# Kernel optimization log

Measured on AMD Instinct MI355X. Metric: run time of the kernel, lower is better.

Reference implementation:

```python
import jax, jax.numpy as jnp
import numpy as np

F = 16  # ConvLSTM2D filters

def hard_sigmoid(x):
    # Keras (TF2) hard_sigmoid: clip(0.2*x + 0.5, 0, 1) -- ConvLSTM2D default recurrent_activation
    return jnp.clip(0.2 * x + 0.5, 0.0, 1.0)

def convlstm_1x1(x, W, U, b, reverse):
    # x: [B,T,H,W,C]; W: [C,4F]; U: [F,4F]; b: [4F]
    # 1x1 ConvLSTM2D == per-pixel LSTM; gate order in Keras kernel: i, f, c, o
    B, T, H, Wd, C = x.shape
    xs = jnp.moveaxis(x, 1, 0)  # [T,B,H,W,C]
    h0 = jnp.zeros((B, H, Wd, F), x.dtype)
    c0 = jnp.zeros((B, H, Wd, F), x.dtype)
    def step(carry, xt):
        h, c = carry
        z = jnp.einsum('bhwc,cf->bhwf', xt, W) + jnp.einsum('bhwc,cf->bhwf', h, U) + b
        i, f, g, o = jnp.split(z, 4, axis=-1)
        i = hard_sigmoid(i); f = hard_sigmoid(f); o = hard_sigmoid(o)
        c_new = f * c + i * jnp.tanh(g)
        h_new = o * jnp.tanh(c_new)
        return (h_new, c_new), h_new
    # reverse=True: scan runs backward in time, ys aligned to input order,
    # which matches Keras Bidirectional(go_backwards + output re-reversal).
    _, hs = jax.lax.scan(step, (h0, c0), xs, reverse=reverse)
    return jnp.moveaxis(hs, 0, 1)  # [B,T,H,W,F]

def setup_inputs() -> dict:
    key = jax.random.key(0)
    ks = jax.random.split(key, 13)
    B, T, H, Wd, C = 16, 64, 32, 32, 32
    s = 0.1
    inp = {
        'inputs': jax.random.normal(ks[0], (B, T, H, Wd, C), jnp.float32),
        'Wf': jax.random.normal(ks[1], (C, 4 * F), jnp.float32) * s,
        'Uf': jax.random.normal(ks[2], (F, 4 * F), jnp.float32) * s,
        'bf': jnp.zeros((4 * F,), jnp.float32),
        'Wb': jax.random.normal(ks[3], (C, 4 * F), jnp.float32) * s,
        'Ub': jax.random.normal(ks[4], (F, 4 * F), jnp.float32) * s,
        'bb': jnp.zeros((4 * F,), jnp.float32),
        'w1': jax.random.normal(ks[5], (2 * F, 16), jnp.float32) * s,
        'b1': jnp.zeros((16,), jnp.float32),
        'w2': jax.random.normal(ks[6], (16, 16), jnp.float32) * s,
        'b2': jnp.zeros((16,), jnp.float32),
        'w3': jax.random.normal(ks[7], (16, 10), jnp.float32) * s,
        'b3': jnp.zeros((10,), jnp.float32),
    }
    return inp

def reference(inputs, Wf, Uf, bf, Wb, Ub, bb, w1, b1, w2, b2, w3, b3):
    h_fwd = convlstm_1x1(inputs, Wf, Uf, bf, reverse=False)
    h_bwd = convlstm_1x1(inputs, Wb, Ub, bb, reverse=True)
    x = jnp.concatenate([h_fwd, h_bwd], axis=-1)  # [B,T,H,W,2F]
    x = jnp.einsum('...c,cd->...d', x, w1) + b1
    x = jnp.einsum('...c,cd->...d', x, w2) + b2
    x = jnp.einsum('...c,cd->...d', x, w3) + b3
    return x  # [B,T,H,W,10]
```

## Files before the change

kernel.cpp:

```cpp
#include <hip/hip_runtime.h>
#include <hip/hip_bf16.h>
#include <cstdint>
#include <cstddef>

#define TT 64
#define CC 32
#define FF 16
#define HWSZ 1024
#define NPIX 16384

typedef __attribute__((ext_vector_type(8))) short  short8;
typedef __attribute__((ext_vector_type(4))) float  f32x4;

__device__ __forceinline__ float bf2f(unsigned int u16) {
  union { unsigned int u; float f; } c;
  c.u = u16 << 16;
  return c.f;
}
__device__ __forceinline__ unsigned int f2bf(float f) {
  union { float f; unsigned int u; } c;
  c.f = f;
  unsigned int u = c.u;
  return (u + 0x7fffu + ((u >> 16) & 1u)) >> 16;
}
__device__ __forceinline__ unsigned int pkbf(float a, float b) {
  float2 f2; f2.x = a; f2.y = b;
  __hip_bfloat162 h = __float22bfloat162_rn(f2);
  union { __hip_bfloat162 h; unsigned int u; } c; c.h = h;
  return c.u;
}
__device__ __forceinline__ float clamp01(float x) {
  return fminf(fmaxf(x, 0.0f), 1.0f);
}

#define L2E2 2.8853900817779268f
__device__ __forceinline__ float tanh_e2(float e2arg) {
  const float e = __builtin_exp2f(e2arg);
  const float t = __builtin_amdgcn_rcpf(e + 1.0f);
  return fmaf(-2.0f, t, 1.0f);
}

__global__ __launch_bounds__(512) void fold_kernel(
    const float* __restrict__ w1, const float* __restrict__ b1,
    const float* __restrict__ w2, const float* __restrict__ b2,
    const float* __restrict__ w3, const float* __restrict__ b3,
    float* __restrict__ Wc, float* __restrict__ bc)
{
  __shared__ float w23[16 * 10];
  __shared__ float bb2[16];
  const int t = threadIdx.x;

  if (t < 160) {
    const int k = t / 10, j = t % 10;
    float s = 0.0f;
    #pragma unroll
    for (int m = 0; m < 16; ++m) s = fmaf(w2[k * 16 + m], w3[m * 10 + j], s);
    w23[t] = s;
  }
  if (t < 16) {
    float s = b2[t];
    #pragma unroll
    for (int m = 0; m < 16; ++m) s = fmaf(b1[m], w2[m * 16 + t], s);
    bb2[t] = s;
  }
  __syncthreads();
  if (t < 320) {
    const int k = t / 10, j = t % 10;
    float s = 0.0f;
    #pragma unroll
    for (int m = 0; m < 16; ++m) s = fmaf(w1[k * 16 + m], w23[m * 10 + j], s);
    Wc[t] = s;
  }
  if (t < 10) {
    float s = b3[t];
    #pragma unroll
    for (int m = 0; m < 16; ++m) s = fmaf(bb2[m], w3[m * 10 + t], s);
    bc[t] = s;
  }
}

__global__ __launch_bounds__(256) void lstm_kernel(
    const float* __restrict__ x,
    const float* __restrict__ Wf, const float* __restrict__ Uf, const float* __restrict__ bfp,
    const float* __restrict__ Wb, const float* __restrict__ Ub, const float* __restrict__ bbp,
    unsigned short* __restrict__ hf_out, unsigned short* __restrict__ hb_out)
{
  const int dir = blockIdx.y;
  const float* __restrict__ Wp = dir ? Wb : Wf;
  const float* __restrict__ Up = dir ? Ub : Uf;
  const float* __restrict__ bp = dir ? bbp : bfp;
  unsigned short* __restrict__ hout = dir ? hb_out : hf_out;

  const int tid  = threadIdx.x;
  const int lane = tid & 63;
  const int wid  = tid >> 6;
  const int quad = lane >> 4;
  const int l15  = lane & 15;

  __shared__ unsigned short hst[4 * 16 * 40];
  unsigned short* hwv = hst + wid * 16 * 40;
  for (int i = tid; i < 4 * 16 * 40; i += 256) hst[i] = 0;
  __syncthreads();

  const int px  = (blockIdx.x * 4 + wid) * 16 + l15;
  const int b   = px >> 10;
  const int hwi = px & 1023;

  short8 Bx[4], Bu[4];
  #pragma unroll
  for (int nt = 0; nt < 4; ++nt) {
    short8 vx, vu;
    #pragma unroll
    for (int j = 0; j < 8; ++j) {
      const int k   = quad * 8 + j;
      const int col = nt * 16 + l15;
      vx[j] = (short)f2bf(Wp[k * 64 + col]);
      vu[j] = (k < FF) ? (short)f2bf(Up[k * 64 + col]) : (short)0;
    }
    Bx[nt] = vx; Bu[nt] = vu;
  }
  const float bi  = fmaf(bp[ 0 + l15], 0.2f, 0.5f);
  const float bf  = fmaf(bp[16 + l15], 0.2f, 0.5f);
  const float bgl = bp[32 + l15] * L2E2;
  const float bo  = fmaf(bp[48 + l15], 0.2f, 0.5f);

  float cst[4] = {0.f, 0.f, 0.f, 0.f};
  const int rd_off = l15 * 40 + quad * 8;

  const int t0 = dir ? (TT - 1) : 0;
  const unsigned int pos0 = (unsigned int)((b * TT + t0) * HWSZ + hwi);
  unsigned int xoff = pos0 * (CC * 4) + quad * 32;
  const int xstep = dir ? -(HWSZ * CC * 4) : (HWSZ * CC * 4);
  unsigned int hob = pos0 * 32 + quad * 16;
  const int hstep = dir ? -(HWSZ * 32) : (HWSZ * 32);
  unsigned int hob_prev = hob;

  const char* xb = (const char*)x;
  char* hbb = (char*)hout;

  float4 x0 = *reinterpret_cast<const float4*>(xb + xoff);
  float4 x1 = *reinterpret_cast<const float4*>(xb + xoff + 16);

  for (int s = 0; s < TT; ++s) {
    union { short8 s8; unsigned int u[4]; } ax;
    ax.u[0] = pkbf(x0.x, x0.y); ax.u[1] = pkbf(x0.z, x0.w);
    ax.u[2] = pkbf(x1.x, x1.y); ax.u[3] = pkbf(x1.z, x1.w);

    if (s + 1 < TT) {
      xoff += xstep;
      x0 = *reinterpret_cast<const float4*>(xb + xoff);
      x1 = *reinterpret_cast<const float4*>(xb + xoff + 16);
    }

    const short8 ah = *reinterpret_cast<const short8*>(hwv + rd_off);

    if (s > 0 && lane < 32) {
      *reinterpret_cast<short8*>(hbb + hob_prev) = ah;
    }

    f32x4 zi = {0.f, 0.f, 0.f, 0.f}, zf = zi, zg = zi, zo = zi;
    zi = __builtin_amdgcn_mfma_f32_16x16x32_bf16(ax.s8, Bx[0], zi, 0, 0, 0);
    zf = __builtin_amdgcn_mfma_f32_16x16x32_bf16(ax.s8, Bx[1], zf, 0, 0, 0);
    zg = __builtin_amdgcn_mfma_f32_16x16x32_bf16(ax.s8, Bx[2], zg, 0, 0, 0);
    zo = __builtin_amdgcn_mfma_f32_16x16x32_bf16(ax.s8, Bx[3], zo, 0, 0, 0);
    zi = __builtin_amdgcn_mfma_f32_16x16x32_bf16(ah, Bu[0], zi, 0, 0, 0);
    zf = __builtin_amdgcn_mfma_f32_16x16x32_bf16(ah, Bu[1], zf, 0, 0, 0);
    zg = __builtin_amdgcn_mfma_f32_16x16x32_bf16(ah, Bu[2], zg, 0, 0, 0);
    zo = __builtin_amdgcn_mfma_f32_16x16x32_bf16(ah, Bu[3], zo, 0, 0, 0);

    float hv[4];
    #pragma unroll
    for (int r = 0; r < 4; ++r) {
      const float ig = clamp01(fmaf(zi[r], 0.2f, bi));
      const float fg = clamp01(fmaf(zf[r], 0.2f, bf));
      const float og = clamp01(fmaf(zo[r], 0.2f, bo));
      const float gg = tanh_e2(fmaf(zg[r], L2E2, bgl));
      cst[r] = fmaf(fg, cst[r], ig * gg);
      hv[r]  = og * tanh_e2(cst[r] * L2E2);
    }
    const unsigned int p01 = pkbf(hv[0], hv[1]);
    const unsigned int p23 = pkbf(hv[2], hv[3]);
    const int wr = quad * 4 * 40 + l15;
    hwv[wr          ] = (unsigned short)(p01 & 0xffffu);
    hwv[wr + 40     ] = (unsigned short)(p01 >> 16);
    hwv[wr + 80     ] = (unsigned short)(p23 & 0xffffu);
    hwv[wr + 120    ] = (unsigned short)(p23 >> 16);

    hob_prev = hob;
    hob += hstep;
  }

  const short8 ahf = *reinterpret_cast<const short8*>(hwv + rd_off);
  if (lane < 32) {
    *reinterpret_cast<short8*>(hbb + hob_prev) = ahf;
  }
}

__global__ __launch_bounds__(256) void dense_kernel(
    const unsigned short* __restrict__ hf, const unsigned short* __restrict__ hb,
    const float* __restrict__ Wc, const float* __restrict__ bc,
    float* __restrict__ out)
{
  const int tid  = threadIdx.x;
  const int lane = tid & 63;
  const int quad = lane >> 4;
  const int l15  = lane & 15;

  short8 Bhi, Blo;
  #pragma unroll
  for (int j = 0; j < 8; ++j) {
    const int k = quad * 8 + j;
    const float v  = (l15 < 10) ? Wc[k * 10 + l15] : 0.0f;
    const unsigned int hi = f2bf(v);
    const float lo = v - bf2f(hi);
    Bhi[j] = (short)hi;
    Blo[j] = (short)f2bf(lo);
  }
  const float bcv = (l15 < 10) ? bc[l15] : 0.0f;

  const unsigned short* __restrict__ src = (quad & 2) ? hb : hf;
  const unsigned int lsub = (quad & 1) * 8;

  const unsigned int gw = (blockIdx.x * 256 + tid) >> 6;

  #pragma unroll
  for (int i = 0; i < 8; ++i) {
    const unsigned int tile  = gw * 8 + i;
    const unsigned int pos16 = tile * 16 + l15;
    const short8 A = *reinterpret_cast<const short8*>(src + pos16 * 16 + lsub);

    f32x4 acc = {bcv, bcv, bcv, bcv};
    acc = __builtin_amdgcn_mfma_f32_16x16x32_bf16(A, Bhi, acc, 0, 0, 0);
    acc = __builtin_amdgcn_mfma_f32_16x16x32_bf16(A, Blo, acc, 0, 0, 0);

    if (l15 < 10) {
      const unsigned int rowbase = tile * 16 + quad * 4;
      #pragma unroll
      for (int r = 0; r < 4; ++r) {
        out[(size_t)(rowbase + r) * 10 + l15] = acc[r];
      }
    }
  }
}

extern "C" void kernel_launch(void* const* d_in, const int* in_sizes, int n_in,
                              void* d_out, int out_size, void* d_ws, size_t ws_size,
                              hipStream_t stream) {
  const float* x   = (const float*)d_in[0];
  const float* Wf  = (const float*)d_in[1];
  const float* Uf  = (const float*)d_in[2];
  const float* bfp = (const float*)d_in[3];
  const float* Wb  = (const float*)d_in[4];
  const float* Ub  = (const float*)d_in[5];
  const float* bbp = (const float*)d_in[6];
  const float* w1  = (const float*)d_in[7];
  const float* b1  = (const float*)d_in[8];
  const float* w2  = (const float*)d_in[9];
  const float* b2  = (const float*)d_in[10];
  const float* w3  = (const float*)d_in[11];
  const float* b3  = (const float*)d_in[12];

  unsigned short* hfbuf = (unsigned short*)d_ws;
  unsigned short* hbbuf = hfbuf + (size_t)NPIX * TT * FF;
  float* Wc = (float*)(hbbuf + (size_t)NPIX * TT * FF);
  float* bc = Wc + 320;

  fold_kernel<<<1, 512, 0, stream>>>(w1, b1, w2, b2, w3, b3, Wc, bc);

  lstm_kernel<<<dim3(256, 2), 256, 0, stream>>>(x, Wf, Uf, bfp, Wb, Ub, bbp, hfbuf, hbbuf);

  dense_kernel<<<2048, 256, 0, stream>>>(hfbuf, hbbuf, Wc, bc, (float*)d_out);
}
```

Baseline: 282.9 us.

## Transpose LSTM MFMA, pass hidden state via bpermute, precompute next input projection

The recurrent kernel now uses the transposed MFMA formulation: the weights are operand A and the pixel vectors are operand B. The hidden state is redistributed between lanes with ds_bpermute instead of a per-wave LDS buffer, which removes the shared-memory stores and loads on every timestep. The input projection for step t+1 is computed off the critical path while step t runs, and x loads are double-buffered two steps ahead. This shortens the serial dependency chain per timestep, at the cost of more registers and more complex indexing.

After: 277.7 us. Within noise of the previous version (-1.8%).

```diff
diff --git a/kernel.cpp b/kernel.cpp
--- a/kernel.cpp
+++ b/kernel.cpp
@@ -97,102 +97,125 @@
   const int quad = lane >> 4;
   const int l15  = lane & 15;
 
-  __shared__ unsigned short hst[4 * 16 * 40];
-  unsigned short* hwv = hst + wid * 16 * 40;
-  for (int i = tid; i < 4 * 16 * 40; i += 256) hst[i] = 0;
-  __syncthreads();
-
   const int px  = (blockIdx.x * 4 + wid) * 16 + l15;
   const int b   = px >> 10;
   const int hwi = px & 1023;
 
-  short8 Bx[4], Bu[4];
+  short8 AW[4], AU[4];
   #pragma unroll
   for (int nt = 0; nt < 4; ++nt) {
-    short8 vx, vu;
+    short8 vw, vu;
     #pragma unroll
     for (int j = 0; j < 8; ++j) {
       const int k   = quad * 8 + j;
       const int col = nt * 16 + l15;
-      vx[j] = (short)f2bf(Wp[k * 64 + col]);
+      vw[j] = (short)f2bf(Wp[k * 64 + col]);
       vu[j] = (k < FF) ? (short)f2bf(Up[k * 64 + col]) : (short)0;
     }
-    Bx[nt] = vx; Bu[nt] = vu;
-  }
-  const float bi  = fmaf(bp[ 0 + l15], 0.2f, 0.5f);
-  const float bf  = fmaf(bp[16 + l15], 0.2f, 0.5f);
-  const float bgl = bp[32 + l15] * L2E2;
-  const float bo  = fmaf(bp[48 + l15], 0.2f, 0.5f);
+    AW[nt] = vw; AU[nt] = vu;
+  }
+
+  float bi[4], bfv[4], bgl[4], bo[4];
+  #pragma unroll
+  for (int r = 0; r < 4; ++r) {
+    const int f = quad * 4 + r;
+    bi[r]  = fmaf(bp[ 0 + f], 0.2f, 0.5f);
+    bfv[r] = fmaf(bp[16 + f], 0.2f, 0.5f);
+    bgl[r] = bp[32 + f] * L2E2;
+    bo[r]  = fmaf(bp[48 + f], 0.2f, 0.5f);
+  }
 
   float cst[4] = {0.f, 0.f, 0.f, 0.f};
-  const int rd_off = l15 * 40 + quad * 8;
+  union BU { short8 s8; int i[4]; };
+  BU Bh; Bh.i[0] = 0; Bh.i[1] = 0; Bh.i[2] = 0; Bh.i[3] = 0;
+
+  const int bp0 = (quad * 32 + l15) * 4;
+  const int bp1 = (quad * 32 + 16 + l15) * 4;
+  const bool kreal = (quad < 2);
 
   const int t0 = dir ? (TT - 1) : 0;
   const unsigned int pos0 = (unsigned int)((b * TT + t0) * HWSZ + hwi);
-  unsigned int xoff = pos0 * (CC * 4) + quad * 32;
   const int xstep = dir ? -(HWSZ * CC * 4) : (HWSZ * CC * 4);
+  const int hstep = dir ? -(HWSZ * 32) : (HWSZ * 32);
   unsigned int hob = pos0 * 32 + quad * 16;
-  const int hstep = dir ? -(HWSZ * 32) : (HWSZ * 32);
-  unsigned int hob_prev = hob;
 
   const char* xb = (const char*)x;
   char* hbb = (char*)hout;
 
-  float4 x0 = *reinterpret_cast<const float4*>(xb + xoff);
-  float4 x1 = *reinterpret_cast<const float4*>(xb + xoff + 16);
-
+  const unsigned int xo0 = pos0 * (CC * 4) + quad * 32;
+  float4 a0 = *reinterpret_cast<const float4*>(xb + xo0);
+  float4 a1 = *reinterpret_cast<const float4*>(xb + xo0 + 16);
+  const unsigned int xo1 = xo0 + xstep;
+  float4 c0 = *reinterpret_cast<const float4*>(xb + xo1);
+  float4 c1 = *reinterpret_cast<const float4*>(xb + xo1 + 16);
+  unsigned int xoffL = xo1 + xstep;
+
+  f32x4 zx[4];
+  {
+    BU ax;
+    ax.i[0] = pkbf(a0.x, a0.y); ax.i[1] = pkbf(a0.z, a0.w);
+    ax.i[2] = pkbf(a1.x, a1.y); ax.i[3] = pkbf(a1.z, a1.w);
+    const f32x4 zz = {0.f, 0.f, 0.f, 0.f};
+    #pragma unroll
+    for (int nt = 0; nt < 4; ++nt)
+      zx[nt] = __builtin_amdgcn_mfma_f32_16x16x32_bf16(AW[nt], ax.s8, zz, 0, 0, 0);
+  }
+  a0 = *reinterpret_cast<const float4*>(xb + xoffL);
+  a1 = *reinterpret_cast<const float4*>(xb + xoffL + 16);
+
+  #pragma unroll 2
   for (int s = 0; s < TT; ++s) {
-    union { short8 s8; unsigned int u[4]; } ax;
-    ax.u[0] = pkbf(x0.x, x0.y); ax.u[1] = pkbf(x0.z, x0.w);
-    ax.u[2] = pkbf(x1.x, x1.y); ax.u[3] = pkbf(x1.z, x1.w);
-
-    if (s + 1 < TT) {
-      xoff += xstep;
-      x0 = *reinterpret_cast<const float4*>(xb + xoff);
-      x1 = *reinterpret_cast<const float4*>(xb + xoff + 16);
-    }
-
-    const short8 ah = *reinterpret_cast<const short8*>(hwv + rd_off);
-
-    if (s > 0 && lane < 32) {
-      *reinterpret_cast<short8*>(hbb + hob_prev) = ah;
-    }
-
-    f32x4 zi = {0.f, 0.f, 0.f, 0.f}, zf = zi, zg = zi, zo = zi;
-    zi = __builtin_amdgcn_mfma_f32_16x16x32_bf16(ax.s8, Bx[0], zi, 0, 0, 0);
-    zf = __builtin_amdgcn_mfma_f32_16x16x32_bf16(ax.s8, Bx[1], zf, 0, 0, 0);
-    zg = __builtin_amdgcn_mfma_f32_16x16x32_bf16(ax.s8, Bx[2], zg, 0, 0, 0);
-    zo = __builtin_amdgcn_mfma_f32_16x16x32_bf16(ax.s8, Bx[3], zo, 0, 0, 0);
-    zi = __builtin_amdgcn_mfma_f32_16x16x32_bf16(ah, Bu[0], zi, 0, 0, 0);
-    zf = __builtin_amdgcn_mfma_f32_16x16x32_bf16(ah, Bu[1], zf, 0, 0, 0);
-    zg = __builtin_amdgcn_mfma_f32_16x16x32_bf16(ah, Bu[2], zg, 0, 0, 0);
-    zo = __builtin_amdgcn_mfma_f32_16x16x32_bf16(ah, Bu[3], zo, 0, 0, 0);
+    f32x4 z[4];
+    #pragma unroll
+    for (int nt = 0; nt < 4; ++nt)
+      z[nt] = __builtin_amdgcn_mfma_f32_16x16x32_bf16(AU[nt], Bh.s8, zx[nt], 0, 0, 0);
+
+    {
+      const float4 u0 = (s & 1) ? a0 : c0;
+      const float4 u1 = (s & 1) ? a1 : c1;
+      BU ax;
+      ax.i[0] = pkbf(u0.x, u0.y); ax.i[1] = pkbf(u0.z, u0.w);
+      ax.i[2] = pkbf(u1.x, u1.y); ax.i[3] = pkbf(u1.z, u1.w);
+      const f32x4 zz = {0.f, 0.f, 0.f, 0.f};
+      #pragma unroll
+      for (int nt = 0; nt < 4; ++nt)
+        zx[nt] = __builtin_amdgcn_mfma_f32_16x16x32_bf16(AW[nt], ax.s8, zz, 0, 0, 0);
+    }
+    if (s + 3 < TT) xoffL += xstep;
+    if (s & 1) {
+      a0 = *reinterpret_cast<const float4*>(xb + xoffL);
+      a1 = *reinterpret_cast<const float4*>(xb + xoffL + 16);
+    } else {
+      c0 = *reinterpret_cast<const float4*>(xb + xoffL);
+      c1 = *reinterpret_cast<const float4*>(xb + xoffL + 16);
+    }
 
     float hv[4];
     #pragma unroll
     for (int r = 0; r < 4; ++r) {
-      const float ig = clamp01(fmaf(zi[r], 0.2f, bi));
-      const float fg = clamp01(fmaf(zf[r], 0.2f, bf));
-      const float og = clamp01(fmaf(zo[r], 0.2f, bo));
-      const float gg = tanh_e2(fmaf(zg[r], L2E2, bgl));
+      const float ig = clamp01(fmaf(z[0][r], 0.2f, bi[r]));
+      const float fg = clamp01(fmaf(z[1][r], 0.2f, bfv[r]));
+      const float og = clamp01(fmaf(z[3][r], 0.2f, bo[r]));
+      const float gg = tanh_e2(fmaf(z[2][r], L2E2, bgl[r]));
       cst[r] = fmaf(fg, cst[r], ig * gg);
       hv[r]  = og * tanh_e2(cst[r] * L2E2);
     }
-    const unsigned int p01 = pkbf(hv[0], hv[1]);
-    const unsigned int p23 = pkbf(hv[2], hv[3]);
-    const int wr = quad * 4 * 40 + l15;
-    hwv[wr          ] = (unsigned short)(p01 & 0xffffu);
-    hwv[wr + 40     ] = (unsigned short)(p01 >> 16);
-    hwv[wr + 80     ] = (unsigned short)(p23 & 0xffffu);
-    hwv[wr + 120    ] = (unsigned short)(p23 >> 16);
-
-    hob_prev = hob;
+
+    const int p01 = (int)pkbf(hv[0], hv[1]);
+    const int p23 = (int)pkbf(hv[2], hv[3]);
+    int d0 = __builtin_amdgcn_ds_bpermute(bp0, p01);
+    int d1 = __builtin_amdgcn_ds_bpermute(bp0, p23);
+    int d2 = __builtin_amdgcn_ds_bpermute(bp1, p01);
+    int d3 = __builtin_amdgcn_ds_bpermute(bp1, p23);
+    Bh.i[0] = kreal ? d0 : 0;
+    Bh.i[1] = kreal ? d1 : 0;
+    Bh.i[2] = kreal ? d2 : 0;
+    Bh.i[3] = kreal ? d3 : 0;
+
+    if (lane < 32) {
+      *reinterpret_cast<short8*>(hbb + hob) = Bh.s8;
+    }
     hob += hstep;
-  }
-
-  const short8 ahf = *reinterpret_cast<const short8*>(hwv + rd_off);
-  if (lane < 32) {
-    *reinterpret_cast<short8*>(hbb + hob_prev) = ahf;
   }
 }
 
```
